# Performance work log

Hardware: AMD Instinct MI355X
Metric: run time of the kernel (lower is better)

## Reference

```python
import jax, jax.numpy as jnp
import numpy as np

N = 400000       # number of non-zero points
C_IN = 64
C_OUT = 64
K = 3            # kernel size per dim -> 27 offsets
S = 1024         # coordinate grid bound; packed key = ((x*S)+y)*S+z < 2^30 fits int32


def _pack(c):
    # linear packing: pack(a+b) == pack(a)+pack(b); injective for coords in [0, S-1]^3
    return (c[..., 0].astype(jnp.int32) * S + c[..., 1]) * S + c[..., 2]


def setup_inputs() -> dict:
    rng = np.random.default_rng(0)
    # unique coordinates in [1, S-2]^3 so coord+offset stays in [0, S-1]^3
    cand = rng.integers(1, S - 1, size=(2 * N, 3), dtype=np.int32)
    keys = (cand[:, 0].astype(np.int64) * S + cand[:, 1]) * S + cand[:, 2]
    _, uidx = np.unique(keys, return_index=True)
    coords = cand[np.sort(uidx)][:N]
    assert coords.shape[0] == N
    # kernel offsets: {-1,0,1}^3 in row-major (minuet layout order)
    r = np.arange(-(K // 2), K // 2 + 1)
    offsets = np.stack(np.meshgrid(r, r, r, indexing='ij'), axis=-1).reshape(-1, 3).astype(np.int32)
    key = jax.random.key(0)
    k1, k2 = jax.random.split(key)
    features = jax.random.normal(k1, (N, C_IN), dtype=jnp.float32)
    kernel = jax.random.normal(k2, (K ** 3, C_IN, C_OUT), dtype=jnp.float32) / np.float32(np.sqrt(C_IN * K ** 3))
    return {
        'features': features,
        'kernel': kernel,
        'coords': jnp.asarray(coords),
        'offsets': jnp.asarray(offsets),
    }


def reference(features, kernel, coords, offsets):
    # Sparse conv with stride=1: outputs live at the same (sorted) coordinates.
    # out_i = sum_k 1[p_j == q_i + delta_k] F_j @ W_k  (gather-GEMM-scatter)
    keys = _pack(coords)                      # [N]
    order = jnp.argsort(keys)                 # build sorted coordinate index
    skeys = keys[order]                       # [N] sorted keys
    sfeat = features[order]                   # [N, C_in]
    n = skeys.shape[0]
    okeys = _pack(offsets)                    # [K^3] packed offsets (linearity of _pack)

    def step(acc, xs):
        ok, Wk = xs                           # scalar key offset, [C_in, C_out]
        qk = skeys + ok                       # query keys = target coord + delta_k
        idx = jnp.clip(jnp.searchsorted(skeys, qk), 0, n - 1)
        valid = skeys[idx] == qk              # kernel-map mask for this offset
        g = jnp.where(valid[:, None], sfeat[idx], 0.0)   # gather
        return acc + g @ Wk, None             # GEMM + scatter(accumulate)

    out0 = jnp.zeros((n, kernel.shape[-1]), dtype=features.dtype)
    out, _ = jax.lax.scan(step, out0, (okeys, kernel))
    return out
```

## Files before the change

kernel.cpp:

```cpp
#include <hip/hip_runtime.h>

#define NBUCK  4096
#define SCAP   256
#define QCHUNK 512
#define WPAD   320
#define WCAP   (QCHUNK + 2 * WPAD + 16)
#define GW     96
#define MCAP   96

typedef __bf16 bf16_t;
typedef bf16_t bf16x8 __attribute__((ext_vector_type(8)));
typedef float  f32x4  __attribute__((ext_vector_type(4)));
typedef unsigned long long u64;

__global__ void k_bin(const int* __restrict__ coords, const float* __restrict__ kern,
                      u64* __restrict__ slot, int* __restrict__ cnt,
                      bf16_t* __restrict__ wf, int N, int nb) {
    if (blockIdx.x >= nb) {
        int tid = (blockIdx.x - nb) * 256 + threadIdx.x;
        int f = tid >> 9, l = (tid >> 3) & 63, j = tid & 7;
        int nt = f >> 1, kt = f & 1;
        int k = kt * 32 + ((l >> 4) * 8) + j;
        int n = nt * 16 + (l & 15);
        wf[tid] = (bf16_t)kern[13 * 4096 + k * 64 + n];
        return;
    }
    __shared__ int sc[768];
    int base3 = blockIdx.x * 768;
    for (int t = threadIdx.x; t < 768; t += 256) {
        int idx = base3 + t;
        sc[t] = (idx < 3 * N) ? coords[idx] : 0;
    }
    __syncthreads();
    int i = blockIdx.x * 256 + threadIdx.x;
    if (i < N) {
        int key = (sc[3 * threadIdx.x] << 20) | (sc[3 * threadIdx.x + 1] << 10) | sc[3 * threadIdx.x + 2];
        int b = key >> 18;
        int pos = atomicAdd(&cnt[b], 1);
        if (pos < SCAP)
            slot[(size_t)b * SCAP + pos] = ((u64)(unsigned)key << 20) | (unsigned)i;
    }
}

__global__ void k_sortp(const int* __restrict__ cnt, const u64* __restrict__ slot,
                        int* __restrict__ skeys, int* __restrict__ sorder) {
    int t = threadIdx.x;
    int vals[16];
    int s = 0;
#pragma unroll
    for (int j = 0; j < 16; ++j) {
        int v = cnt[t * 16 + j];
        if (v > SCAP) v = SCAP;
        vals[j] = v; s += v;
    }
    int lane = t & 63, wv = t >> 6;
    int x = s;
#pragma unroll
    for (int d = 1; d < 64; d <<= 1) {
        int y = __shfl_up(x, d, 64);
        if (lane >= d) x += y;
    }
    __shared__ int wsum[4];
    if (lane == 63) wsum[wv] = x;
    __syncthreads();
    int add = 0;
    for (int u = 0; u < wv; ++u) add += wsum[u];
    int run = (x + add) - s;
    __shared__ int sbase[5];
    int b0 = blockIdx.x * 4;
#pragma unroll
    for (int j = 0; j < 16; ++j) {
        int bb = t * 16 + j;
        int d = bb - b0;
        if (d >= 0 && d <= 4) sbase[d] = run;
        run += vals[j];
    }
    if (t == 255 && b0 + 4 == NBUCK) sbase[4] = x + add;
    __syncthreads();

    __shared__ u64 sk[4][SCAP];
    int b = b0 + wv;
    int lo = sbase[wv];
    int size = sbase[wv + 1] - sbase[wv];
    for (int e = lane; e < size; e += 64) sk[wv][e] = slot[(size_t)b * SCAP + e];
    __syncthreads();
    for (int e = lane; e < size; e += 64) {
        u64 my = sk[wv][e];
        int r = 0;
        for (int j = 0; j < size; ++j) r += (sk[wv][j] < my);
        skeys[lo + r]  = (int)(my >> 20);
        sorder[lo + r] = (int)(my & 0xFFFFF);
    }
}

__device__ __forceinline__ int lower_bound_g(const int* __restrict__ a, int n, int q) {
    int lo = 0, hi = n;
    while (lo < hi) { int mid = (lo + hi) >> 1; if (a[mid] < q) lo = mid + 1; else hi = mid; }
    return lo;
}

__global__ __launch_bounds__(256) void k_conv(const int* __restrict__ skeys,
                                              const int* __restrict__ sorder,
                                              const int* __restrict__ offs,
                                              const float* __restrict__ feat,
                                              const bf16_t* __restrict__ wf,
                                              const float* __restrict__ kern,
                                              float* __restrict__ out, int N) {
    const int tid = threadIdx.x;
    const int lane = tid & 63, wv = tid >> 6;
    const int i0 = blockIdx.x * QCHUNK;
    const int iend = min(i0 + QCHUNK, N);

    __shared__ int sw[WCAP];
    __shared__ int mlist[MCAP * 3];
    __shared__ int mcount;
    if (tid == 0) mcount = 0;

    int kq[QCHUNK / 256];
#pragma unroll
    for (int u = 0; u < QCHUNK / 256; ++u) {
        int i = i0 + u * 256 + tid;
        kq[u] = (i < iend) ? skeys[i] : 0;
    }

    for (int g = 0; g < 9; ++g) {
        int kb = 3 * g;
        int ok1 = offs[3 * kb] * 1048576 + offs[3 * kb + 1] * 1024 + offs[3 * kb + 2];
        long long drift = ((long long)ok1 * N) >> 30;
        int wlo = (int)max(0LL, (long long)i0 + drift - WPAD);
        int whi = (int)min((long long)N, (long long)iend + drift + WPAD);
        int wn = whi - wlo;
        __syncthreads();
        for (int t = tid; t < wn; t += 256) sw[t] = skeys[wlo + t];
        __syncthreads();
        int wfirst = sw[0], wlast = sw[wn - 1];

#pragma unroll
        for (int u = 0; u < QCHUNK / 256; ++u) {
            int i = i0 + u * 256 + tid;
            if (i >= iend) continue;
            int q1 = kq[u] + ok1;
            if (q1 >= wfirst && q1 + 2 <= wlast) {
                int p = (int)((long long)i + drift) - wlo;
                p = min(max(p, 0), wn - 1);
                int L = max(p - GW, 0), H = min(p + GW, wn - 1);
                if (!(sw[L] < q1 && sw[H] >= q1)) { L = 0; H = wn - 1; }
                while (L < H) { int mid = (L + H) >> 1; if (sw[mid] < q1) L = mid + 1; else H = mid; }
                int pos = L;
#pragma unroll
                for (int t3 = 0; t3 < 3; ++t3) {
                    if (g == 4 && t3 == 1) { if (sw[pos] == q1 + 1) pos++; continue; }
                    if (sw[pos] == q1 + t3) {
                        int tk = atomicAdd(&mcount, 1);
                        if (tk < MCAP) {
                            mlist[3 * tk]     = i;
                            mlist[3 * tk + 1] = sorder[wlo + pos];
                            mlist[3 * tk + 2] = kb + t3;
                        }
                        pos++;
                    }
                }
            } else {
                for (int t3 = 0; t3 < 3; ++t3) {
                    if (g == 4 && t3 == 1) continue;
                    int qt = q1 + t3;
                    if (qt < wfirst && wlo == 0) continue;
                    if (qt > wlast && whi == N) continue;
                    int j = -1;
                    if (qt >= wfirst && qt <= wlast) {
                        int L = 0, H = wn - 1;
                        while (L < H) { int mid = (L + H) >> 1; if (sw[mid] < qt) L = mid + 1; else H = mid; }
                        if (sw[L] == qt) j = wlo + L;
                    } else {
                        int pos = lower_bound_g(skeys, N, qt);
                        if (pos < N && skeys[pos] == qt) j = pos;
                    }
                    if (j >= 0) {
                        int tk = atomicAdd(&mcount, 1);
                        if (tk < MCAP) {
                            mlist[3 * tk] = i; mlist[3 * tk + 1] = sorder[j]; mlist[3 * tk + 2] = kb + t3;
                        }
                    }
                }
            }
        }
    }

    const int m = lane & 15, quad = lane >> 4;
    for (int s = 0; s < QCHUNK / 64; ++s) {
        int tile = i0 + s * 64 + wv * 16;
        int srow = tile + m;
        int gi = (srow < N) ? srow : N - 1;
        int orig = sorder[gi];
        const float* rp = feat + (size_t)orig * 64;
        bf16x8 a[2];
#pragma unroll
        for (int kt = 0; kt < 2; ++kt) {
            const float* p = rp + kt * 32 + quad * 8;
            float4 x = *(const float4*)p;
            float4 y = *(const float4*)(p + 4);
            bf16x8 v;
            v[0] = (bf16_t)x.x; v[1] = (bf16_t)x.y; v[2] = (bf16_t)x.z; v[3] = (bf16_t)x.w;
            v[4] = (bf16_t)y.x; v[5] = (bf16_t)y.y; v[6] = (bf16_t)y.z; v[7] = (bf16_t)y.w;
            a[kt] = v;
        }
#pragma unroll
        for (int nt = 0; nt < 4; ++nt) {
            f32x4 acc = {0.f, 0.f, 0.f, 0.f};
#pragma unroll
            for (int kt = 0; kt < 2; ++kt) {
                bf16x8 bfr = *(const bf16x8*)(wf + ((nt * 2 + kt) * 64 + lane) * 8);
                acc = __builtin_amdgcn_mfma_f32_16x16x32_bf16(a[kt], bfr, acc, 0, 0, 0);
            }
#pragma unroll
            for (int r = 0; r < 4; ++r) {
                int orow = tile + quad * 4 + r;
                if (orow < iend) out[(size_t)orow * 64 + nt * 16 + m] = acc[r];
            }
        }
    }
    __syncthreads();

    int ntask = min(mcount, MCAP);
    for (int t = wv; t < ntask; t += 4) {
        int dst = mlist[3 * t], src = mlist[3 * t + 1], wk = mlist[3 * t + 2];
        float f = feat[(size_t)src * 64 + lane];
        const float* W = kern + wk * 4096;
        float acc = 0.f;
#pragma unroll
        for (int cc = 0; cc < 64; ++cc)
            acc += __shfl(f, cc, 64) * W[cc * 64 + lane];
        atomicAdd(&out[(size_t)dst * 64 + lane], acc);
    }
}

extern "C" void kernel_launch(void* const* d_in, const int* in_sizes, int n_in,
                              void* d_out, int out_size, void* d_ws, size_t ws_size,
                              hipStream_t stream) {
    const float* feat   = (const float*)d_in[0];
    const float* kern   = (const float*)d_in[1];
    const int*   coords = (const int*)d_in[2];
    const int*   offs   = (const int*)d_in[3];
    float* out = (float*)d_out;
    int N = in_sizes[0] / 64;

    char* w = (char*)d_ws;
    auto alloc = [&](size_t bytes) { char* p = w; w += (bytes + 255) & ~(size_t)255; return p; };
    u64* slot    = (u64*)alloc((size_t)NBUCK * SCAP * 8);
    int* skeys   = (int*)alloc((size_t)N * 4);
    int* sorder  = (int*)alloc((size_t)N * 4);
    int* cnt     = (int*)alloc(NBUCK * 4);
    bf16_t* wf   = (bf16_t*)alloc(4096 * 2);

    hipMemsetAsync(cnt, 0, NBUCK * 4, stream);

    int nb  = (N + 255) / 256;
    int nch = (N + QCHUNK - 1) / QCHUNK;
    k_bin  <<<nb + 16, 256, 0, stream>>>(coords, kern, slot, cnt, wf, N, nb);
    k_sortp<<<NBUCK / 4, 256, 0, stream>>>(cnt, slot, skeys, sorder);
    k_conv <<<nch, 256, 0, stream>>>(skeys, sorder, offs, feat, wf, kern, out, N);
}
```

Baseline: 277.9 us.

## Search kernel map per x-slab with one range scan; alternate phase order across blocks

The kernel-map search now does one binary search per x-offset for the lower key of a 3x3 y/z neighbourhood and linearly scans the sorted window up to the upper key, decoding dy/dz from each key difference. This replaces nine windowed searches with three, and three window loads into shared memory instead of nine. It also swaps the order of the search phase and the center-offset MFMA phase on odd blocks, so that memory-bound and compute phases overlap across blocks. The cost is a variable-length scan per query, which can diverge across lanes, plus a global fallback path that does up to nine full binary searches.

```diff
diff --git a/kernel.cpp b/kernel.cpp
--- a/kernel.cpp
+++ b/kernel.cpp
@@ -5,7 +5,6 @@
 #define QCHUNK 512
 #define WPAD   320
 #define WCAP   (QCHUNK + 2 * WPAD + 16)
-#define GW     96
 #define MCAP   96
 
 typedef __bf16 bf16_t;
@@ -123,102 +122,103 @@
         kq[u] = (i < iend) ? skeys[i] : 0;
     }
 
-    for (int g = 0; g < 9; ++g) {
-        int kb = 3 * g;
-        int ok1 = offs[3 * kb] * 1048576 + offs[3 * kb + 1] * 1024 + offs[3 * kb + 2];
-        long long drift = ((long long)ok1 * N) >> 30;
-        int wlo = (int)max(0LL, (long long)i0 + drift - WPAD);
-        int whi = (int)min((long long)N, (long long)iend + drift + WPAD);
-        int wn = whi - wlo;
-        __syncthreads();
-        for (int t = tid; t < wn; t += 256) sw[t] = skeys[wlo + t];
-        __syncthreads();
-        int wfirst = sw[0], wlast = sw[wn - 1];
-
-#pragma unroll
-        for (int u = 0; u < QCHUNK / 256; ++u) {
-            int i = i0 + u * 256 + tid;
-            if (i >= iend) continue;
-            int q1 = kq[u] + ok1;
-            if (q1 >= wfirst && q1 + 2 <= wlast) {
-                int p = (int)((long long)i + drift) - wlo;
-                p = min(max(p, 0), wn - 1);
-                int L = max(p - GW, 0), H = min(p + GW, wn - 1);
-                if (!(sw[L] < q1 && sw[H] >= q1)) { L = 0; H = wn - 1; }
-                while (L < H) { int mid = (L + H) >> 1; if (sw[mid] < q1) L = mid + 1; else H = mid; }
-                int pos = L;
-#pragma unroll
-                for (int t3 = 0; t3 < 3; ++t3) {
-                    if (g == 4 && t3 == 1) { if (sw[pos] == q1 + 1) pos++; continue; }
-                    if (sw[pos] == q1 + t3) {
+    auto phaseA = [&]() {
+        for (int w = 0; w < 3; ++w) {
+            const int dx = w - 1;
+            const int okdx = dx << 20;
+            const long long drift = ((long long)okdx * N) >> 30;
+            const int gw = (dx == 0) ? 16 : 96;
+            int wlo = (int)max(0LL, (long long)i0 + drift - WPAD);
+            int whi = (int)min((long long)N, (long long)iend + drift + WPAD);
+            int wn = whi - wlo;
+            __syncthreads();
+            for (int t = tid; t < wn; t += 256) sw[t] = skeys[wlo + t];
+            __syncthreads();
+            int wfirst = sw[0], wlast = sw[wn - 1];
+
+#pragma unroll
+            for (int u = 0; u < QCHUNK / 256; ++u) {
+                int i = i0 + u * 256 + tid;
+                if (i >= iend) continue;
+                int q0 = kq[u] + okdx;
+                int lok = q0 - 1025, hik = q0 + 1025;
+                if (lok > wfirst && hik < wlast) {
+                    int p = (int)((long long)i + drift) - wlo;
+                    p = min(max(p, 0), wn - 1);
+                    int L = max(p - gw, 0), H = min(p + gw, wn - 1);
+                    if (!(sw[L] < lok && sw[H] >= lok)) { L = 0; H = wn - 1; }
+                    while (L < H) { int mid = (L + H) >> 1; if (sw[mid] < lok) L = mid + 1; else H = mid; }
+                    for (int pos = L; sw[pos] <= hik; ++pos) {
+                        int d = sw[pos] - q0;
+                        if (d == 0 && dx == 0) continue;
+                        int dy, dz;
+                        if (d >= -1 && d <= 1)            { dy = 0;  dz = d; }
+                        else if (d >= 1023 && d <= 1025)  { dy = 1;  dz = d - 1024; }
+                        else if (d >= -1025 && d <= -1023){ dy = -1; dz = d + 1024; }
+                        else continue;
+                        int kk = (dx + 1) * 9 + (dy + 1) * 3 + (dz + 1);
                         int tk = atomicAdd(&mcount, 1);
                         if (tk < MCAP) {
-                            mlist[3 * tk]     = i;
-                            mlist[3 * tk + 1] = sorder[wlo + pos];
-                            mlist[3 * tk + 2] = kb + t3;
-                        }
-                        pos++;
-                    }
-                }
-            } else {
-                for (int t3 = 0; t3 < 3; ++t3) {
-                    if (g == 4 && t3 == 1) continue;
-                    int qt = q1 + t3;
-                    if (qt < wfirst && wlo == 0) continue;
-                    if (qt > wlast && whi == N) continue;
-                    int j = -1;
-                    if (qt >= wfirst && qt <= wlast) {
-                        int L = 0, H = wn - 1;
-                        while (L < H) { int mid = (L + H) >> 1; if (sw[mid] < qt) L = mid + 1; else H = mid; }
-                        if (sw[L] == qt) j = wlo + L;
-                    } else {
-                        int pos = lower_bound_g(skeys, N, qt);
-                        if (pos < N && skeys[pos] == qt) j = pos;
-                    }
-                    if (j >= 0) {
-                        int tk = atomicAdd(&mcount, 1);
-                        if (tk < MCAP) {
-                            mlist[3 * tk] = i; mlist[3 * tk + 1] = sorder[j]; mlist[3 * tk + 2] = kb + t3;
+                            mlist[3 * tk] = i; mlist[3 * tk + 1] = sorder[wlo + pos]; mlist[3 * tk + 2] = kk;
                         }
                     }
+                } else {
+                    for (int dy = -1; dy <= 1; ++dy)
+                        for (int dz = -1; dz <= 1; ++dz) {
+                            if (dx == 0 && dy == 0 && dz == 0) continue;
+                            int qt = q0 + dy * 1024 + dz;
+                            int pos = lower_bound_g(skeys, N, qt);
+                            if (pos < N && skeys[pos] == qt) {
+                                int kk = (dx + 1) * 9 + (dy + 1) * 3 + (dz + 1);
+                                int tk = atomicAdd(&mcount, 1);
+                                if (tk < MCAP) {
+                                    mlist[3 * tk] = i; mlist[3 * tk + 1] = sorder[pos]; mlist[3 * tk + 2] = kk;
+                                }
+                            }
+                        }
                 }
             }
         }
-    }
-
-    const int m = lane & 15, quad = lane >> 4;
-    for (int s = 0; s < QCHUNK / 64; ++s) {
-        int tile = i0 + s * 64 + wv * 16;
-        int srow = tile + m;
-        int gi = (srow < N) ? srow : N - 1;
-        int orig = sorder[gi];
-        const float* rp = feat + (size_t)orig * 64;
-        bf16x8 a[2];
-#pragma unroll
-        for (int kt = 0; kt < 2; ++kt) {
-            const float* p = rp + kt * 32 + quad * 8;
-            float4 x = *(const float4*)p;
-            float4 y = *(const float4*)(p + 4);
-            bf16x8 v;
-            v[0] = (bf16_t)x.x; v[1] = (bf16_t)x.y; v[2] = (bf16_t)x.z; v[3] = (bf16_t)x.w;
-            v[4] = (bf16_t)y.x; v[5] = (bf16_t)y.y; v[6] = (bf16_t)y.z; v[7] = (bf16_t)y.w;
-            a[kt] = v;
-        }
-#pragma unroll
-        for (int nt = 0; nt < 4; ++nt) {
-            f32x4 acc = {0.f, 0.f, 0.f, 0.f};
+    };
+
+    auto phaseB = [&]() {
+        const int m = lane & 15, quad = lane >> 4;
+        for (int s = 0; s < QCHUNK / 64; ++s) {
+            int tile = i0 + s * 64 + wv * 16;
+            int srow = tile + m;
+            int gi = (srow < N) ? srow : N - 1;
+            int orig = sorder[gi];
+            const float* rp = feat + (size_t)orig * 64;
+            bf16x8 a[2];
 #pragma unroll
             for (int kt = 0; kt < 2; ++kt) {
-                bf16x8 bfr = *(const bf16x8*)(wf + ((nt * 2 + kt) * 64 + lane) * 8);
-                acc = __builtin_amdgcn_mfma_f32_16x16x32_bf16(a[kt], bfr, acc, 0, 0, 0);
+                const float* p = rp + kt * 32 + quad * 8;
+                float4 x = *(const float4*)p;
+                float4 y = *(const float4*)(p + 4);
+                bf16x8 v;
+                v[0] = (bf16_t)x.x; v[1] = (bf16_t)x.y; v[2] = (bf16_t)x.z; v[3] = (bf16_t)x.w;
+                v[4] = (bf16_t)y.x; v[5] = (bf16_t)y.y; v[6] = (bf16_t)y.z; v[7] = (bf16_t)y.w;
+                a[kt] = v;
             }
 #pragma unroll
-            for (int r = 0; r < 4; ++r) {
-                int orow = tile + quad * 4 + r;
-                if (orow < iend) out[(size_t)orow * 64 + nt * 16 + m] = acc[r];
+            for (int nt = 0; nt < 4; ++nt) {
+                f32x4 acc = {0.f, 0.f, 0.f, 0.f};
+#pragma unroll
+                for (int kt = 0; kt < 2; ++kt) {
+                    bf16x8 bfr = *(const bf16x8*)(wf + ((nt * 2 + kt) * 64 + lane) * 8);
+                    acc = __builtin_amdgcn_mfma_f32_16x16x32_bf16(a[kt], bfr, acc, 0, 0, 0);
+                }
+#pragma unroll
+                for (int r = 0; r < 4; ++r) {
+                    int orow = tile + quad * 4 + r;
+                    if (orow < iend) out[(size_t)orow * 64 + nt * 16 + m] = acc[r];
+                }
             }
         }
-    }
+    };
+
+    if (blockIdx.x & 1) { phaseB(); phaseA(); }
+    else                { phaseA(); phaseB(); }
     __syncthreads();
 
     int ntask = min(mcount, MCAP);
```

Result: slower. 310.1 us (+11.6%).
